# Kernel optimization log

Hardware: AMD Instinct MI355X
Metric: run time of the kernel (lower is better)

## Reference

```python
import math
import jax, jax.numpy as jnp
import numpy as np

N_MARKS = 64
D_TYPE = 256      # d_type_emb (= d_k since each head module has n_head=1)
D_TIME = 256      # must be even
N_HEAD = 4
N_LAYERS = 3
D_IN = D_TYPE + D_TIME  # input dim to per-layer QKV projections
NEG = -1000000000.0
LN_EPS = 1e-5


def temporal_embedding(time):
    # time: [B,T] -> [B,T,D_TIME]; pe[...,0::2]=sin(t*div), pe[...,1::2]=cos(t*div)
    div_term = jnp.exp(jnp.arange(0, D_TIME, 2, dtype=time.dtype) * (-(math.log(10000.0) / D_TIME)))
    ang = time[..., None] * div_term  # [B,T,D_TIME//2]
    pe = jnp.stack([jnp.sin(ang), jnp.cos(ang)], axis=-1)  # interleave sin/cos
    return pe.reshape(time.shape[0], time.shape[1], D_TIME)


def layer_norm(x, w, b):
    mu = jnp.mean(x, axis=-1, keepdims=True)
    var = jnp.mean(jnp.square(x - mu), axis=-1, keepdims=True)
    return (x - mu) * jax.lax.rsqrt(var + LN_EPS) * w + b


def setup_inputs() -> dict:
    key = jax.random.key(0)
    ks = jax.random.split(key, 12)
    B, T = 4, 1024
    event_seqs = jax.random.uniform(ks[0], (B, T, N_MARKS), dtype=jnp.float32)
    time_seqs = jax.random.uniform(ks[1], (B, T), dtype=jnp.float32)
    non_pad_mask = jnp.ones((B, T, T), dtype=bool)
    s_in = 1.0 / math.sqrt(D_IN)
    s_mk = 1.0 / math.sqrt(N_MARKS)
    Wtype = jax.random.uniform(ks[2], (N_MARKS, D_TYPE), minval=-s_mk, maxval=s_mk)
    btype = jax.random.uniform(ks[3], (D_TYPE,), minval=-s_mk, maxval=s_mk)
    Wq = jax.random.uniform(ks[4], (N_HEAD, N_LAYERS, D_IN, D_TYPE), minval=-s_in, maxval=s_in)
    bq = jax.random.uniform(ks[5], (N_HEAD, N_LAYERS, D_TYPE), minval=-s_in, maxval=s_in)
    Wk = jax.random.uniform(ks[6], (N_HEAD, N_LAYERS, D_IN, D_TYPE), minval=-s_in, maxval=s_in)
    bk = jax.random.uniform(ks[7], (N_HEAD, N_LAYERS, D_TYPE), minval=-s_in, maxval=s_in)
    Wv = jax.random.uniform(ks[8], (N_HEAD, N_LAYERS, D_IN, D_TYPE), minval=-s_in, maxval=s_in)
    bv = jax.random.uniform(ks[9], (N_HEAD, N_LAYERS, D_TYPE), minval=-s_in, maxval=s_in)
    norm_w = jnp.ones((D_TYPE,), dtype=jnp.float32)
    norm_b = jnp.zeros((D_TYPE,), dtype=jnp.float32)
    return {"event_seqs": event_seqs, "time_seqs": time_seqs, "non_pad_mask": non_pad_mask,
            "Wtype": Wtype, "btype": btype, "Wq": Wq, "bq": bq, "Wk": Wk, "bk": bk,
            "Wv": Wv, "bv": bv, "norm_w": norm_w, "norm_b": norm_b}


def reference(event_seqs, time_seqs, non_pad_mask, Wtype, btype, Wq, bq, Wk, bk, Wv, bv, norm_w, norm_b):
    B, T, _ = event_seqs.shape
    # attention mask: True => masked (torch masked_fill(mask > 0, -1e9)); strict+diag upper tri
    tri = jnp.triu(jnp.ones((T, T), dtype=bool))[None]           # [1,T,T]
    attention_mask = tri & non_pad_mask                          # [B,T,T]
    layer_mask = jnp.broadcast_to(~jnp.eye(T, dtype=bool)[None], (B, T, T))
    top = jnp.concatenate([attention_mask, jnp.ones((B, T, T), dtype=bool)], axis=-1)
    bot = jnp.concatenate([attention_mask, layer_mask], axis=-1)
    combined_mask = jnp.concatenate([top, bot], axis=1)          # [B,2T,2T]

    time_emb = temporal_embedding(time_seqs)                     # [B,T,D_TIME]
    type_emb = jnp.tanh(event_seqs @ Wtype + btype)              # [B,T,D_TYPE]
    event_emb = jnp.concatenate([type_emb, time_emb], axis=-1)   # [B,T,D_IN]
    sample_time_emb = time_emb                                   # sample_times=None path
    init_cur = jnp.zeros_like(type_emb)

    scale = 1.0 / math.sqrt(D_TYPE)
    cur_layers = []
    # NOTE: event_emb is sequentially updated across layers AND heads, matching the source.
    for h in range(N_HEAD):
        cur = init_cur
        for l in range(N_LAYERS):
            x = jnp.concatenate([event_emb,
                                 jnp.concatenate([cur, sample_time_emb], axis=-1)], axis=1)  # [B,2T,D_IN]
            q = x @ Wq[h, l] + bq[h, l]
            k = x @ Wk[h, l] + bk[h, l]
            v = x @ Wv[h, l] + bv[h, l]
            scores = jnp.einsum('bqd,bkd->bqk', q, k) * scale    # [B,2T,2T]
            scores = jnp.where(combined_mask, NEG, scores)
            p = jax.nn.softmax(scores, axis=-1)
            out = jnp.einsum('bqk,bkd->bqd', p, v)               # [B,2T,D_TYPE]
            cur = jnp.tanh(out[:, T:, :]) + cur
            event_emb = jnp.concatenate([out[:, :T, :], time_emb], axis=-1)
            cur = layer_norm(cur, norm_w, norm_b)                # use_norm=True
        cur_layers.append(cur)
    return jnp.concatenate(cur_layers, axis=-1)                  # [B,T,D_TYPE*N_HEAD]
```

## Files before the change

### kernel.cpp

```cpp
#include <hip/hip_runtime.h>

typedef __attribute__((ext_vector_type(8))) short short8;
typedef __attribute__((ext_vector_type(4))) float f32x4;
typedef __attribute__((ext_vector_type(4))) unsigned short us4v;
typedef unsigned short ushort_t;
typedef unsigned int uint_t;

#define BB 4
#define T_ 1024
#define T2 2048
#define DD 256
#define DIN 512
#define NMARK 64
#define LNEPS 1e-5f
#define KDIV (-0.035977892078032f)
#define SEGL 8

__device__ __forceinline__ ushort_t f2bf(float f) {
  unsigned int u = __float_as_uint(f);
  unsigned int r = (u + 0x7fffu + ((u >> 16) & 1u)) >> 16;
  return (ushort_t)r;
}
__device__ __forceinline__ uint_t pack2(float a, float b) {
  return (uint_t)f2bf(a) | ((uint_t)f2bf(b) << 16);
}
__device__ __forceinline__ uint_t cvtpk(float lo, float hi) {
  uint_t r;
  asm("v_cvt_pk_bf16_f32 %0, %1, %2" : "=v"(r) : "v"(lo), "v"(hi));
  return r;
}

typedef const __attribute__((address_space(1))) unsigned int* as1cu32;
typedef __attribute__((address_space(3))) unsigned int* as3u32;
__device__ __forceinline__ void async_copy16(const void* g, void* l) {
  __builtin_amdgcn_global_load_lds((as1cu32)g, (as3u32)l, 16, 0, 0);
}

__global__ __launch_bounds__(256) void k_init(const float* __restrict__ ev,
                                              const float* __restrict__ tm,
                                              const float* __restrict__ Wt,
                                              const float* __restrict__ bt,
                                              ushort_t* __restrict__ Xh,
                                              float* __restrict__ Cur) {
  const int btq = blockIdx.x;
  const int b = btq >> 10;
  const int t = btq & 1023;
  const int d = threadIdx.x;
  __shared__ float evs[NMARK];
  if (d < NMARK) evs[d] = ev[(size_t)btq * NMARK + d];
  __syncthreads();
  float s = bt[d];
#pragma unroll
  for (int m = 0; m < NMARK; ++m) s += evs[m] * Wt[m * DD + d];
  const float te_type = tanhf(s);
  const float tv = tm[btq];
  const int i = d >> 1;
  const float dv = expf((float)(2 * i) * KDIV);
  const float ang = tv * dv;
  const float te_time = (d & 1) ? cosf(ang) : sinf(ang);
  ushort_t* Xb = Xh + (size_t)b * T2 * DIN;
  const ushort_t tt = f2bf(te_time);
  Xb[(size_t)t * DIN + d] = f2bf(te_type);
  Xb[(size_t)t * DIN + DD + d] = tt;
  Xb[(size_t)(T_ + t) * DIN + d] = 0;
  Xb[(size_t)(T_ + t) * DIN + DD + d] = tt;
  Cur[((size_t)b * T_ + t) * DD + d] = 0.0f;
}

__global__ __launch_bounds__(256) void k_transW(const float* __restrict__ Wq,
                                                const float* __restrict__ Wk,
                                                const float* __restrict__ Wv,
                                                ushort_t* __restrict__ WT) {
  const int mi = blockIdx.x;
  const int wsel = mi / 12, hl = mi % 12;
  const float* W = ((wsel == 0) ? Wq : (wsel == 1) ? Wk : Wv) + (size_t)hl * DIN * DD;
  const int t = blockIdx.y;
  const int k0 = (t >> 2) * 64, n0 = (t & 3) * 64;
  __shared__ float Ts[64][65];
  const int tid = threadIdx.x;
#pragma unroll
  for (int i = 0; i < 16; ++i) {
    const int idx = tid + i * 256;
    const int r = idx >> 6, c = idx & 63;
    Ts[r][c] = W[(size_t)(k0 + r) * DD + n0 + c];
  }
  __syncthreads();
  ushort_t* D = WT + (size_t)mi * DD * DIN;
#pragma unroll
  for (int i = 0; i < 16; ++i) {
    const int idx = tid + i * 256;
    const int rn = idx >> 6, ck = idx & 63;
    D[(size_t)(n0 + rn) * DIN + k0 + ck] = f2bf(Ts[ck][rn]);
  }
}

__global__ __launch_bounds__(256) void k_qkv(const ushort_t* __restrict__ Xh,
                                             const ushort_t* __restrict__ WT,
                                             const float* __restrict__ bq,
                                             const float* __restrict__ bk,
                                             const float* __restrict__ bv,
                                             ushort_t* __restrict__ Qh,
                                             ushort_t* __restrict__ Kh,
                                             ushort_t* __restrict__ VTt,
                                             int hl) {
  const int m0 = blockIdx.x * 128;
  const int n0 = blockIdx.y * 128;
  const int wsel = blockIdx.z;
  const ushort_t* Bt = WT + ((size_t)(wsel * 12 + hl)) * DD * DIN + (size_t)n0 * DIN;
  const float* bias = (wsel == 0) ? bq : (wsel == 1) ? bk : bv;

  __shared__ ushort_t As[128 * 64];
  __shared__ ushort_t Bs[128 * 64];
  const int tid = threadIdx.x;
  const int w = tid >> 6, lane = tid & 63;
  const int wr = w >> 1, wc = w & 1;
  const int lr = lane & 15, kg = lane >> 4;

  f32x4 acc[4][4];
  const f32x4 z4 = {0.f, 0.f, 0.f, 0.f};
#pragma unroll
  for (int a = 0; a < 4; ++a)
#pragma unroll
    for (int c = 0; c < 4; ++c) acc[a][c] = z4;

  for (int k0 = 0; k0 < DIN; k0 += 64) {
#pragma unroll
    for (int i = 0; i < 4; ++i) {
      const int idx = tid + i * 256;
      const int row = idx >> 3, ch = idx & 7;
      const int db = row * 128 + ((ch * 16) ^ ((row & 7) << 4));
      uint4 va = *(const uint4*)&Xh[(size_t)(m0 + row) * DIN + k0 + ch * 8];
      *(uint4*)((char*)As + db) = va;
      uint4 vb = *(const uint4*)&Bt[(size_t)row * DIN + k0 + ch * 8];
      *(uint4*)((char*)Bs + db) = vb;
    }
    __syncthreads();
#pragma unroll
    for (int kk = 0; kk < 2; ++kk) {
      short8 af[4], bfr[4];
      const int cb = kk * 64 + kg * 16;
#pragma unroll
      for (int mi = 0; mi < 4; ++mi) {
        const int row = wr * 64 + mi * 16 + lr;
        af[mi] = *(const short8*)((const char*)As + row * 128 + (cb ^ ((row & 7) << 4)));
      }
#pragma unroll
      for (int ni = 0; ni < 4; ++ni) {
        const int row = wc * 64 + ni * 16 + lr;
        bfr[ni] = *(const short8*)((const char*)Bs + row * 128 + (cb ^ ((row & 7) << 4)));
      }
#pragma unroll
      for (int mi = 0; mi < 4; ++mi)
#pragma unroll
        for (int ni = 0; ni < 4; ++ni)
          acc[mi][ni] = __builtin_amdgcn_mfma_f32_16x16x32_bf16(af[mi], bfr[ni], acc[mi][ni], 0, 0, 0);
    }
    __syncthreads();
  }

  if (wsel < 2) {
    ushort_t* C = (wsel == 0) ? Qh : Kh;
#pragma unroll
    for (int mi = 0; mi < 4; ++mi)
#pragma unroll
      for (int ni = 0; ni < 4; ++ni) {
        const int col = n0 + wc * 64 + ni * 16 + lr;
        const float bcol = bias[col];
        const int rbase = m0 + wr * 64 + mi * 16 + kg * 4;
#pragma unroll
        for (int r = 0; r < 4; ++r)
          C[(size_t)(rbase + r) * DD + col] = f2bf(acc[mi][ni][r] + bcol);
      }
  } else {
    const int b2 = m0 >> 11;
    const int t0q = m0 & 2047;
#pragma unroll
    for (int mi = 0; mi < 4; ++mi)
#pragma unroll
      for (int ni = 0; ni < 4; ++ni) {
        const int col = n0 + wc * 64 + ni * 16 + lr;
        const float bcol = bias[col];
        const int t32 = (t0q >> 5) + wr * 2 + (mi >> 1);
        const int jloc = kg * 8 + (mi & 1) * 4;
        uint2 pk;
        pk.x = pack2(acc[mi][ni][0] + bcol, acc[mi][ni][1] + bcol);
        pk.y = pack2(acc[mi][ni][2] + bcol, acc[mi][ni][3] + bcol);
        *(uint2*)(VTt + ((size_t)(b2 * 64 + t32)) * (DD * 32) + col * 32 + jloc) = pk;
      }
  }
}

__global__ __launch_bounds__(128, 1) void k_fpart(const ushort_t* __restrict__ Qh,
                                                  const ushort_t* __restrict__ Kh,
                                                  const ushort_t* __restrict__ VTt,
                                                  float* __restrict__ PartO,
                                                  float* __restrict__ PartML) {
  __shared__ char lds[65536];
  const int tid = threadIdx.x;
  const int bx = blockIdx.x;
  const int r = bx & 255;
  const int seg = bx >> 8;
  const int hb = r & 1;
  const int b = (r >> 1) & 3;
  const int tc = 31 - (r >> 3);
  const int nt = tc + 1 + hb;
  const int nseg = (nt + SEGL - 1) / SEGL;
  if (seg >= nseg) return;
  const int kt0 = seg * SEGL;
  const int klen = (nt - kt0 < SEGL) ? (nt - kt0) : SEGL;
  const int t0 = tc * 32;
  const int nc = tc + 1;
  const int dt = 32 + tc;

  const int w = tid >> 6, lane = tid & 63;
  const int kg = lane >> 4, lr = lane & 15;
  const int tloc = w * 16 + lr;
  const int t = t0 + tloc;
  const int r0 = (hb ? T_ : 0) + t;
  const size_t bT2 = (size_t)b * T2;

  short8 qf[8];
  {
    const ushort_t* qb = Qh + (bT2 + r0) * DD + kg * 8;
#pragma unroll
    for (int kk = 0; kk < 8; ++kk) qf[kk] = *(const short8*)(qb + kk * 32);
  }

  const f32x4 z4 = {0.f, 0.f, 0.f, 0.f};
  f32x4 acc_o[16];
#pragma unroll
  for (int db = 0; db < 16; ++db) acc_o[db] = z4;
  float m_run = -1e30f, l_run = 0.f;

#define STAGE(BUF, TILE)                                                                  \
  {                                                                                       \
    const int _t = (TILE);                                                                \
    const char* Vt = (const char*)VTt + ((size_t)(b * 64 + _t)) * 16384;                  \
    _Pragma("unroll") for (int s = 0; s < 8; ++s) {                                       \
      const int row2 = (w * 8 + s) * 2 + (lane >> 5);                                     \
      const int cc2 = lane & 31;                                                          \
      async_copy16((const char*)Kh + ((bT2 + _t * 32 + row2) * DD) * 2 +                  \
                       ((cc2 * 16) ^ ((row2 & 7) << 4)),                                  \
                   lds + (BUF) * 16384 + (w * 8 + s) * 1024);                             \
      async_copy16(Vt + (w * 8 + s) * 1024 + (lane << 4),                                 \
                   lds + 32768 + (BUF) * 16384 + (w * 8 + s) * 1024);                     \
    }                                                                                     \
  }
#define TILEOF(KT) (((KT) < nc) ? (KT) : dt)

  STAGE(0, TILEOF(kt0));

  union U8 { uint4 u; short8 s; };

  for (int ktl = 0; ktl < klen; ++ktl) {
    const int kt = kt0 + ktl;
    const int tile = TILEOF(kt);
    const bool isDiag = (kt >= nc);

    if (ktl + 1 < klen) {
      STAGE((ktl + 1) & 1, TILEOF(kt + 1));
      asm volatile("s_waitcnt vmcnt(16)" ::: "memory");
    } else {
      asm volatile("s_waitcnt vmcnt(0)" ::: "memory");
    }
    __builtin_amdgcn_s_barrier();
    asm volatile("" ::: "memory");

    const char* KsC = lds + (ktl & 1) * 16384;
    const char* VsC = lds + 32768 + (ktl & 1) * 16384;

    f32x4 sa[2];
#pragma unroll
    for (int jb = 0; jb < 2; ++jb) {
      sa[jb] = z4;
      const int rowj = jb * 16 + lr;
      const int base = rowj * 512;
      const int swj = (rowj & 7) << 4;
#pragma unroll
      for (int kk = 0; kk < 8; ++kk) {
        short8 kf = *(const short8*)(KsC + base + ((kk * 64 + kg * 16) ^ swj));
        sa[jb] = __builtin_amdgcn_mfma_f32_16x16x32_bf16(kf, qf[kk], sa[jb], 0, 0, 0);
      }
    }

    float sv[8];
    float tmax = -1e30f;
#pragma unroll
    for (int jb = 0; jb < 2; ++jb)
#pragma unroll
      for (int rr = 0; rr < 4; ++rr) {
        const int jl = jb * 16 + kg * 4 + rr;
        const bool valid = isDiag ? (jl == tloc) : ((tile * 32 + jl) < t);
        const float x = valid ? sa[jb][rr] * 0.0625f : -1e30f;
        sv[jb * 4 + rr] = x;
        tmax = fmaxf(tmax, x);
      }
    tmax = fmaxf(tmax, __shfl_xor(tmax, 16, 64));
    tmax = fmaxf(tmax, __shfl_xor(tmax, 32, 64));
    if (tmax > m_run + 8.0f) {
      const float fac = __expf(m_run - tmax);
      m_run = tmax;
      l_run *= fac;
#pragma unroll
      for (int db = 0; db < 16; ++db) acc_o[db] *= fac;
    }
    float p[8];
    float psum = 0.f;
#pragma unroll
    for (int e = 0; e < 8; ++e) {
      const float pe = (sv[e] > -1e29f) ? __expf(sv[e] - m_run) : 0.0f;
      p[e] = pe;
      psum += pe;
    }
    psum += __shfl_xor(psum, 16, 64);
    psum += __shfl_xor(psum, 32, 64);
    l_run += psum;

    U8 pf;
    pf.u.x = cvtpk(p[0], p[1]);
    pf.u.y = cvtpk(p[2], p[3]);
    pf.u.z = cvtpk(p[4], p[5]);
    pf.u.w = cvtpk(p[6], p[7]);

#pragma unroll
    for (int db = 0; db < 16; ++db) {
      U8 vf;
      vf.u = *(const uint4*)(VsC + (db * 16 + lr) * 64 + kg * 16);
      acc_o[db] = __builtin_amdgcn_mfma_f32_16x16x32_bf16(vf.s, pf.s, acc_o[db], 0, 0, 0);
    }

    __builtin_amdgcn_s_barrier();
    asm volatile("" ::: "memory");
  }
#undef STAGE
#undef TILEOF

  float* pml = PartML + (r * 5 + seg) * 64;
  if (kg == 0) { pml[tloc] = m_run; pml[32 + tloc] = l_run; }
  float* po = PartO + ((size_t)(r * 5 + seg)) * (32 * 256) + tloc * 256 + kg * 4;
#pragma unroll
  for (int db = 0; db < 16; ++db) *(f32x4*)(po + db * 16) = acc_o[db];
}

__global__ __launch_bounds__(128) void k_merge(const ushort_t* __restrict__ VTt,
                                               float* __restrict__ Cur,
                                               ushort_t* __restrict__ Xh,
                                               float* __restrict__ out,
                                               const float* __restrict__ nw,
                                               const float* __restrict__ nb,
                                               const float* __restrict__ PartO,
                                               const float* __restrict__ PartML,
                                               int lastLayer, int h) {
  __shared__ float red[128];
  const int tid = threadIdx.x;
  const int r = blockIdx.x;
  const int hb = r & 1;
  const int b = (r >> 1) & 3;
  const int tc = 31 - (r >> 3);
  const int nt = tc + 1 + hb;
  const int nseg = (nt + SEGL - 1) / SEGL;
  const int t0 = tc * 32;

  const int w = tid >> 6, lane = tid & 63;
  const int kg = lane >> 4, lr = lane & 15;
  const int tloc = w * 16 + lr;
  const int t = t0 + tloc;
  const size_t bT2 = (size_t)b * T2;
  const f32x4 z4 = {0.f, 0.f, 0.f, 0.f};

  float mstar = -1e30f;
  for (int s = 0; s < nseg; ++s)
    mstar = fmaxf(mstar, PartML[(r * 5 + s) * 64 + tloc]);
  float l_run = 0.f;
  f32x4 acc_o[16];
#pragma unroll
  for (int db = 0; db < 16; ++db) acc_o[db] = z4;
  for (int s = 0; s < nseg; ++s) {
    const float* pml = PartML + (r * 5 + s) * 64;
    const float f = __expf(pml[tloc] - mstar);
    l_run += f * pml[32 + tloc];
    const float* po = PartO + ((size_t)(r * 5 + s)) * (32 * 256) + tloc * 256 + kg * 4;
#pragma unroll
    for (int db = 0; db < 16; ++db) {
      f32x4 v = *(const f32x4*)(po + db * 16);
#pragma unroll
      for (int q = 0; q < 4; ++q) acc_o[db][q] += f * v[q];
    }
  }

  const float oinv = 1.0f / l_run;

  if (!hb) {
    if (t != 0) {
      ushort_t* xp = Xh + (bT2 + t) * DIN + kg * 4;
#pragma unroll
      for (int db = 0; db < 16; ++db) {
        us4v o;
#pragma unroll
        for (int rr = 0; rr < 4; ++rr) o[rr] = f2bf(acc_o[db][rr] * oinv);
        *(us4v*)(xp + db * 16) = o;
      }
    }
  } else {
    float* cp = Cur + ((size_t)b * T_ + t) * DD + kg * 4;
    float s1 = 0.f, s2 = 0.f;
#pragma unroll
    for (int db = 0; db < 16; ++db) {
      f32x4 c4 = *(const f32x4*)(cp + db * 16);
#pragma unroll
      for (int rr = 0; rr < 4; ++rr) {
        const float x = tanhf(acc_o[db][rr] * oinv) + c4[rr];
        acc_o[db][rr] = x;
        s1 += x;
        s2 += x * x;
      }
    }
    s1 += __shfl_xor(s1, 16, 64); s1 += __shfl_xor(s1, 32, 64);
    s2 += __shfl_xor(s2, 16, 64); s2 += __shfl_xor(s2, 32, 64);
    const float mean = s1 * (1.0f / 256.0f);
    const float var = s2 * (1.0f / 256.0f) - mean * mean;
    const float rinv = rsqrtf(var + LNEPS);
    ushort_t* xp = Xh + (bT2 + T_ + t) * DIN + kg * 4;
    if (lastLayer) {
      float* op = out + ((size_t)b * T_ + t) * (DD * 4) + h * DD + kg * 4;
      const us4v zz = {0, 0, 0, 0};
      const f32x4 zf = {0.f, 0.f, 0.f, 0.f};
#pragma unroll
      for (int db = 0; db < 16; ++db) {
        f32x4 w4 = *(const f32x4*)&nw[db * 16 + kg * 4];
        f32x4 b4 = *(const f32x4*)&nb[db * 16 + kg * 4];
        f32x4 y;
#pragma unroll
        for (int rr = 0; rr < 4; ++rr) y[rr] = (acc_o[db][rr] - mean) * rinv * w4[rr] + b4[rr];
        *(f32x4*)(op + db * 16) = y;
        *(f32x4*)(cp + db * 16) = zf;
        *(us4v*)(xp + db * 16) = zz;
      }
    } else {
#pragma unroll
      for (int db = 0; db < 16; ++db) {
        f32x4 w4 = *(const f32x4*)&nw[db * 16 + kg * 4];
        f32x4 b4 = *(const f32x4*)&nb[db * 16 + kg * 4];
        f32x4 y;
        us4v yh;
#pragma unroll
        for (int rr = 0; rr < 4; ++rr) {
          y[rr] = (acc_o[db][rr] - mean) * rinv * w4[rr] + b4[rr];
          yh[rr] = f2bf(y[rr]);
        }
        *(f32x4*)(cp + db * 16) = y;
        *(us4v*)(xp + db * 16) = yh;
      }
    }
  }

  if (!hb && tc < 4) {
    const int col = tc * 64 + (tid & 63);
    const int half = tid >> 6;
    float s = 0.f;
    for (int tl = half * 32; tl < half * 32 + 32; ++tl) {
      const ushort_t* vp = VTt + ((size_t)(b * 64 + tl)) * 8192 + col * 32;
#pragma unroll
      for (int j = 0; j < 32; j += 8) {
        uint4 v = *(const uint4*)(vp + j);
        const uint_t vs[4] = {v.x, v.y, v.z, v.w};
#pragma unroll
        for (int q = 0; q < 4; ++q) {
          s += __uint_as_float(vs[q] << 16);
          s += __uint_as_float(vs[q] & 0xffff0000u);
        }
      }
    }
    red[half * 64 + (tid & 63)] = s;
    __syncthreads();
    if (tid < 64)
      Xh[bT2 * DIN + tc * 64 + tid] =
          f2bf((red[tid] + red[64 + tid]) * (1.0f / 2048.0f));
  }
}

extern "C" void kernel_launch(void* const* d_in, const int* in_sizes, int n_in,
                              void* d_out, int out_size, void* d_ws, size_t ws_size,
                              hipStream_t stream) {
  const float* ev = (const float*)d_in[0];
  const float* tm = (const float*)d_in[1];
  const float* Wt = (const float*)d_in[3];
  const float* bt = (const float*)d_in[4];
  const float* Wq = (const float*)d_in[5];
  const float* bq = (const float*)d_in[6];
  const float* Wk = (const float*)d_in[7];
  const float* bk = (const float*)d_in[8];
  const float* Wv = (const float*)d_in[9];
  const float* bv = (const float*)d_in[10];
  const float* nw = (const float*)d_in[11];
  const float* nb = (const float*)d_in[12];
  float* out = (float*)d_out;

  char* p = (char*)d_ws;
  ushort_t* Xh  = (ushort_t*)p; p += (size_t)BB * T2 * DIN * 2;
  ushort_t* Qh  = (ushort_t*)p; p += (size_t)BB * T2 * DD * 2;
  ushort_t* Kh  = (ushort_t*)p; p += (size_t)BB * T2 * DD * 2;
  ushort_t* VTt = (ushort_t*)p; p += (size_t)BB * T2 * DD * 2;
  float* Cur    = (float*)p;    p += (size_t)BB * T_ * DD * 4;
  ushort_t* WT  = (ushort_t*)p; p += (size_t)36 * DD * DIN * 2;
  float* PartO  = (float*)p;    p += (size_t)256 * 5 * 32 * 256 * 4;
  float* PartML = (float*)p;

  k_init<<<BB * T_, 256, 0, stream>>>(ev, tm, Wt, bt, Xh, Cur);
  k_transW<<<dim3(36, 32), 256, 0, stream>>>(Wq, Wk, Wv, WT);

  for (int h = 0; h < 4; ++h) {
    for (int l = 0; l < 3; ++l) {
      const int hl = h * 3 + l;
      const size_t boff = (size_t)hl * DD;
      k_qkv<<<dim3(64, 2, 3), 256, 0, stream>>>(Xh, WT, bq + boff, bk + boff, bv + boff,
                                                Qh, Kh, VTt, hl);
      k_fpart<<<1280, 128, 0, stream>>>(Qh, Kh, VTt, PartO, PartML);
      k_merge<<<256, 128, 0, stream>>>(VTt, Cur, Xh, out, nw, nb,
                                       PartO, PartML, (l == 2) ? 1 : 0, h);
    }
  }
}
```

Before: 783.8 us.

## Share K/V tiles across both query halves and fuse single-segment epilogue into attention

Each attention block now covers the event half and the sample half of the same 32-row query chunk with 4 waves, so each staged K/V tile in LDS is loaded once and used by both halves. The event-half waves skip the diagonal tile. Blocks that need only one key segment finish the tanh/layernorm epilogue inline, which removes the partial-result writes and the merge work for short rows. The merge kernel now runs only on chunks with several segments. The larger blocks and the epilogue code inside the attention kernel may raise register pressure and reduce occupancy.

```diff
diff --git a/kernel.cpp b/kernel.cpp
--- a/kernel.cpp
+++ b/kernel.cpp
@@ -190,33 +190,37 @@
   }
 }
 
-__global__ __launch_bounds__(128, 1) void k_fpart(const ushort_t* __restrict__ Qh,
+__global__ __launch_bounds__(256, 2) void k_fpart(const ushort_t* __restrict__ Qh,
                                                   const ushort_t* __restrict__ Kh,
                                                   const ushort_t* __restrict__ VTt,
+                                                  float* __restrict__ Cur,
+                                                  ushort_t* __restrict__ Xh,
+                                                  float* __restrict__ out,
+                                                  const float* __restrict__ nw,
+                                                  const float* __restrict__ nb,
                                                   float* __restrict__ PartO,
-                                                  float* __restrict__ PartML) {
-  __shared__ char lds[65536];
+                                                  float* __restrict__ PartML,
+                                                  int lastLayer, int h) {
+  __shared__ char lds[66560];
   const int tid = threadIdx.x;
   const int bx = blockIdx.x;
-  const int r = bx & 255;
-  const int seg = bx >> 8;
-  const int hb = r & 1;
-  const int b = (r >> 1) & 3;
-  const int tc = 31 - (r >> 3);
-  const int nt = tc + 1 + hb;
+  const int seg = bx >> 7;
+  const int rem = bx & 127;
+  const int b = rem & 3;
+  const int tc = 31 - (rem >> 2);
+  const int nt = tc + 2;
   const int nseg = (nt + SEGL - 1) / SEGL;
   if (seg >= nseg) return;
   const int kt0 = seg * SEGL;
   const int klen = (nt - kt0 < SEGL) ? (nt - kt0) : SEGL;
-  const int t0 = tc * 32;
-  const int nc = tc + 1;
   const int dt = 32 + tc;
 
   const int w = tid >> 6, lane = tid & 63;
   const int kg = lane >> 4, lr = lane & 15;
-  const int tloc = w * 16 + lr;
-  const int t = t0 + tloc;
-  const int r0 = (hb ? T_ : 0) + t;
+  const int half = w >> 1;
+  const int tq = (w & 1) * 16 + lr;
+  const int t = tc * 32 + tq;
+  const int r0 = (half ? T_ : 0) + t;
   const size_t bT2 = (size_t)b * T2;
 
   short8 qf[8];
@@ -236,17 +240,18 @@
   {                                                                                       \
     const int _t = (TILE);                                                                \
     const char* Vt = (const char*)VTt + ((size_t)(b * 64 + _t)) * 16384;                  \
-    _Pragma("unroll") for (int s = 0; s < 8; ++s) {                                       \
-      const int row2 = (w * 8 + s) * 2 + (lane >> 5);                                     \
+    _Pragma("unroll") for (int s = 0; s < 4; ++s) {                                       \
+      const int c = w * 4 + s;                                                            \
+      const int row2 = (c << 1) | (lane >> 5);                                            \
       const int cc2 = lane & 31;                                                          \
       async_copy16((const char*)Kh + ((bT2 + _t * 32 + row2) * DD) * 2 +                  \
                        ((cc2 * 16) ^ ((row2 & 7) << 4)),                                  \
-                   lds + (BUF) * 16384 + (w * 8 + s) * 1024);                             \
-      async_copy16(Vt + (w * 8 + s) * 1024 + (lane << 4),                                 \
-                   lds + 32768 + (BUF) * 16384 + (w * 8 + s) * 1024);                     \
+                   lds + (BUF) * 16384 + c * 1024);                                       \
+      async_copy16(Vt + c * 1024 + lane * 16,                                             \
+                   lds + 32768 + (BUF) * 16384 + c * 1024);                               \
     }                                                                                     \
   }
-#define TILEOF(KT) (((KT) < nc) ? (KT) : dt)
+#define TILEOF(KT) (((KT) <= tc) ? (KT) : dt)
 
   STAGE(0, TILEOF(kt0));
 
@@ -255,78 +260,80 @@
   for (int ktl = 0; ktl < klen; ++ktl) {
     const int kt = kt0 + ktl;
     const int tile = TILEOF(kt);
-    const bool isDiag = (kt >= nc);
+    const bool isDiag = (kt > tc);
 
     if (ktl + 1 < klen) {
       STAGE((ktl + 1) & 1, TILEOF(kt + 1));
-      asm volatile("s_waitcnt vmcnt(16)" ::: "memory");
+      asm volatile("s_waitcnt vmcnt(8)" ::: "memory");
     } else {
       asm volatile("s_waitcnt vmcnt(0)" ::: "memory");
     }
     __builtin_amdgcn_s_barrier();
     asm volatile("" ::: "memory");
 
-    const char* KsC = lds + (ktl & 1) * 16384;
-    const char* VsC = lds + 32768 + (ktl & 1) * 16384;
-
-    f32x4 sa[2];
-#pragma unroll
-    for (int jb = 0; jb < 2; ++jb) {
-      sa[jb] = z4;
-      const int rowj = jb * 16 + lr;
-      const int base = rowj * 512;
-      const int swj = (rowj & 7) << 4;
-#pragma unroll
-      for (int kk = 0; kk < 8; ++kk) {
-        short8 kf = *(const short8*)(KsC + base + ((kk * 64 + kg * 16) ^ swj));
-        sa[jb] = __builtin_amdgcn_mfma_f32_16x16x32_bf16(kf, qf[kk], sa[jb], 0, 0, 0);
-      }
-    }
-
-    float sv[8];
-    float tmax = -1e30f;
-#pragma unroll
-    for (int jb = 0; jb < 2; ++jb)
-#pragma unroll
-      for (int rr = 0; rr < 4; ++rr) {
-        const int jl = jb * 16 + kg * 4 + rr;
-        const bool valid = isDiag ? (jl == tloc) : ((tile * 32 + jl) < t);
-        const float x = valid ? sa[jb][rr] * 0.0625f : -1e30f;
-        sv[jb * 4 + rr] = x;
-        tmax = fmaxf(tmax, x);
-      }
-    tmax = fmaxf(tmax, __shfl_xor(tmax, 16, 64));
-    tmax = fmaxf(tmax, __shfl_xor(tmax, 32, 64));
-    if (tmax > m_run + 8.0f) {
-      const float fac = __expf(m_run - tmax);
-      m_run = tmax;
-      l_run *= fac;
-#pragma unroll
-      for (int db = 0; db < 16; ++db) acc_o[db] *= fac;
-    }
-    float p[8];
-    float psum = 0.f;
-#pragma unroll
-    for (int e = 0; e < 8; ++e) {
-      const float pe = (sv[e] > -1e29f) ? __expf(sv[e] - m_run) : 0.0f;
-      p[e] = pe;
-      psum += pe;
-    }
-    psum += __shfl_xor(psum, 16, 64);
-    psum += __shfl_xor(psum, 32, 64);
-    l_run += psum;
-
-    U8 pf;
-    pf.u.x = cvtpk(p[0], p[1]);
-    pf.u.y = cvtpk(p[2], p[3]);
-    pf.u.z = cvtpk(p[4], p[5]);
-    pf.u.w = cvtpk(p[6], p[7]);
-
-#pragma unroll
-    for (int db = 0; db < 16; ++db) {
-      U8 vf;
-      vf.u = *(const uint4*)(VsC + (db * 16 + lr) * 64 + kg * 16);
-      acc_o[db] = __builtin_amdgcn_mfma_f32_16x16x32_bf16(vf.s, pf.s, acc_o[db], 0, 0, 0);
+    if (!(isDiag && half == 0)) {
+      const char* KsC = lds + (ktl & 1) * 16384;
+      const char* VsC = lds + 32768 + (ktl & 1) * 16384;
+
+      f32x4 sa[2];
+#pragma unroll
+      for (int jb = 0; jb < 2; ++jb) {
+        sa[jb] = z4;
+        const int rowj = jb * 16 + lr;
+        const int base = rowj * 512;
+        const int swj = (rowj & 7) << 4;
+#pragma unroll
+        for (int kk = 0; kk < 8; ++kk) {
+          short8 kf = *(const short8*)(KsC + base + ((kk * 64 + kg * 16) ^ swj));
+          sa[jb] = __builtin_amdgcn_mfma_f32_16x16x32_bf16(kf, qf[kk], sa[jb], 0, 0, 0);
+        }
+      }
+
+      float sv[8];
+      float tmax = -1e30f;
+#pragma unroll
+      for (int jb = 0; jb < 2; ++jb)
+#pragma unroll
+        for (int rr = 0; rr < 4; ++rr) {
+          const int jl = jb * 16 + kg * 4 + rr;
+          const bool valid = isDiag ? (jl == tq) : ((tile * 32 + jl) < t);
+          const float x = valid ? sa[jb][rr] * 0.0625f : -1e30f;
+          sv[jb * 4 + rr] = x;
+          tmax = fmaxf(tmax, x);
+        }
+      tmax = fmaxf(tmax, __shfl_xor(tmax, 16, 64));
+      tmax = fmaxf(tmax, __shfl_xor(tmax, 32, 64));
+      if (tmax > m_run + 8.0f) {
+        const float fac = __expf(m_run - tmax);
+        m_run = tmax;
+        l_run *= fac;
+#pragma unroll
+        for (int db = 0; db < 16; ++db) acc_o[db] *= fac;
+      }
+      float p[8];
+      float psum = 0.f;
+#pragma unroll
+      for (int e = 0; e < 8; ++e) {
+        const float pe = (sv[e] > -1e29f) ? __expf(sv[e] - m_run) : 0.0f;
+        p[e] = pe;
+        psum += pe;
+      }
+      psum += __shfl_xor(psum, 16, 64);
+      psum += __shfl_xor(psum, 32, 64);
+      l_run += psum;
+
+      U8 pf;
+      pf.u.x = cvtpk(p[0], p[1]);
+      pf.u.y = cvtpk(p[2], p[3]);
+      pf.u.z = cvtpk(p[4], p[5]);
+      pf.u.w = cvtpk(p[6], p[7]);
+
+#pragma unroll
+      for (int db = 0; db < 16; ++db) {
+        U8 vf;
+        vf.u = *(const uint4*)(VsC + (db * 16 + lr) * 64 + kg * 16);
+        acc_o[db] = __builtin_amdgcn_mfma_f32_16x16x32_bf16(vf.s, pf.s, acc_o[db], 0, 0, 0);
+      }
     }
 
     __builtin_amdgcn_s_barrier();
@@ -335,62 +342,20 @@
 #undef STAGE
 #undef TILEOF
 
-  float* pml = PartML + (r * 5 + seg) * 64;
-  if (kg == 0) { pml[tloc] = m_run; pml[32 + tloc] = l_run; }
-  float* po = PartO + ((size_t)(r * 5 + seg)) * (32 * 256) + tloc * 256 + kg * 4;
-#pragma unroll
-  for (int db = 0; db < 16; ++db) *(f32x4*)(po + db * 16) = acc_o[db];
-}
-
-__global__ __launch_bounds__(128) void k_merge(const ushort_t* __restrict__ VTt,
-                                               float* __restrict__ Cur,
-                                               ushort_t* __restrict__ Xh,
-                                               float* __restrict__ out,
-                                               const float* __restrict__ nw,
-                                               const float* __restrict__ nb,
-                                               const float* __restrict__ PartO,
-                                               const float* __restrict__ PartML,
-                                               int lastLayer, int h) {
-  __shared__ float red[128];
-  const int tid = threadIdx.x;
-  const int r = blockIdx.x;
-  const int hb = r & 1;
-  const int b = (r >> 1) & 3;
-  const int tc = 31 - (r >> 3);
-  const int nt = tc + 1 + hb;
-  const int nseg = (nt + SEGL - 1) / SEGL;
-  const int t0 = tc * 32;
-
-  const int w = tid >> 6, lane = tid & 63;
-  const int kg = lane >> 4, lr = lane & 15;
-  const int tloc = w * 16 + lr;
-  const int t = t0 + tloc;
-  const size_t bT2 = (size_t)b * T2;
-  const f32x4 z4 = {0.f, 0.f, 0.f, 0.f};
-
-  float mstar = -1e30f;
-  for (int s = 0; s < nseg; ++s)
-    mstar = fmaxf(mstar, PartML[(r * 5 + s) * 64 + tloc]);
-  float l_run = 0.f;
-  f32x4 acc_o[16];
-#pragma unroll
-  for (int db = 0; db < 16; ++db) acc_o[db] = z4;
-  for (int s = 0; s < nseg; ++s) {
-    const float* pml = PartML + (r * 5 + s) * 64;
-    const float f = __expf(pml[tloc] - mstar);
-    l_run += f * pml[32 + tloc];
-    const float* po = PartO + ((size_t)(r * 5 + s)) * (32 * 256) + tloc * 256 + kg * 4;
-#pragma unroll
-    for (int db = 0; db < 16; ++db) {
-      f32x4 v = *(const f32x4*)(po + db * 16);
-#pragma unroll
-      for (int q = 0; q < 4; ++q) acc_o[db][q] += f * v[q];
-    }
+  if (nseg > 1) {
+    const int slot = (b * 32 + tc) * 5 + seg;
+    const int row = half * 32 + tq;
+    float* pml = PartML + slot * 128;
+    if (kg == 0) { pml[row] = m_run; pml[64 + row] = l_run; }
+    float* po = PartO + ((size_t)slot) * (64 * 256) + row * 256 + kg * 4;
+#pragma unroll
+    for (int db = 0; db < 16; ++db) *(f32x4*)(po + db * 16) = acc_o[db];
+    return;
   }
 
   const float oinv = 1.0f / l_run;
 
-  if (!hb) {
+  if (!half) {
     if (t != 0) {
       ushort_t* xp = Xh + (bT2 + t) * DIN + kg * 4;
 #pragma unroll
@@ -454,11 +419,13 @@
     }
   }
 
-  if (!hb && tc < 4) {
+  if (tc < 4) {
+    __syncthreads();
+    float* red = (float*)(lds + 65536);
     const int col = tc * 64 + (tid & 63);
-    const int half = tid >> 6;
+    const int q4 = tid >> 6;
     float s = 0.f;
-    for (int tl = half * 32; tl < half * 32 + 32; ++tl) {
+    for (int tl = q4 * 16; tl < q4 * 16 + 16; ++tl) {
       const ushort_t* vp = VTt + ((size_t)(b * 64 + tl)) * 8192 + col * 32;
 #pragma unroll
       for (int j = 0; j < 32; j += 8) {
@@ -471,11 +438,121 @@
         }
       }
     }
-    red[half * 64 + (tid & 63)] = s;
+    red[q4 * 64 + (tid & 63)] = s;
     __syncthreads();
     if (tid < 64)
       Xh[bT2 * DIN + tc * 64 + tid] =
-          f2bf((red[tid] + red[64 + tid]) * (1.0f / 2048.0f));
+          f2bf((red[tid] + red[64 + tid] + red[128 + tid] + red[192 + tid]) * (1.0f / 2048.0f));
+  }
+}
+
+__global__ __launch_bounds__(256) void k_merge(float* __restrict__ Cur,
+                                               ushort_t* __restrict__ Xh,
+                                               float* __restrict__ out,
+                                               const float* __restrict__ nw,
+                                               const float* __restrict__ nb,
+                                               const float* __restrict__ PartO,
+                                               const float* __restrict__ PartML,
+                                               int lastLayer, int h) {
+  const int tid = threadIdx.x;
+  const int bx = blockIdx.x;
+  const int b = bx & 3;
+  const int tc = 7 + (bx >> 2);
+  const int nt = tc + 2;
+  const int nseg = (nt + SEGL - 1) / SEGL;
+  const int slot0 = (b * 32 + tc) * 5;
+
+  const int w = tid >> 6, lane = tid & 63;
+  const int kg = lane >> 4, lr = lane & 15;
+  const int half = w >> 1;
+  const int tq = (w & 1) * 16 + lr;
+  const int t = tc * 32 + tq;
+  const int row = half * 32 + tq;
+  const size_t bT2 = (size_t)b * T2;
+  const f32x4 z4 = {0.f, 0.f, 0.f, 0.f};
+
+  float mstar = -1e30f;
+  for (int s = 0; s < nseg; ++s)
+    mstar = fmaxf(mstar, PartML[(slot0 + s) * 128 + row]);
+  float l_run = 0.f;
+  f32x4 acc_o[16];
+#pragma unroll
+  for (int db = 0; db < 16; ++db) acc_o[db] = z4;
+  for (int s = 0; s < nseg; ++s) {
+    const float* pml = PartML + (slot0 + s) * 128;
+    const float f = __expf(pml[row] - mstar);
+    l_run += f * pml[64 + row];
+    const float* po = PartO + ((size_t)(slot0 + s)) * (64 * 256) + row * 256 + kg * 4;
+#pragma unroll
+    for (int db = 0; db < 16; ++db) {
+      f32x4 v = *(const f32x4*)(po + db * 16);
+#pragma unroll
+      for (int q = 0; q < 4; ++q) acc_o[db][q] += f * v[q];
+    }
+  }
+
+  const float oinv = 1.0f / l_run;
+
+  if (!half) {
+    ushort_t* xp = Xh + (bT2 + t) * DIN + kg * 4;
+#pragma unroll
+    for (int db = 0; db < 16; ++db) {
+      us4v o;
+#pragma unroll
+      for (int rr = 0; rr < 4; ++rr) o[rr] = f2bf(acc_o[db][rr] * oinv);
+      *(us4v*)(xp + db * 16) = o;
+    }
+  } else {
+    float* cp = Cur + ((size_t)b * T_ + t) * DD + kg * 4;
+    float s1 = 0.f, s2 = 0.f;
+#pragma unroll
+    for (int db = 0; db < 16; ++db) {
+      f32x4 c4 = *(const f32x4*)(cp + db * 16);
+#pragma unroll
+      for (int rr = 0; rr < 4; ++rr) {
+        const float x = tanhf(acc_o[db][rr] * oinv) + c4[rr];
+        acc_o[db][rr] = x;
+        s1 += x;
+        s2 += x * x;
+      }
+    }
+    s1 += __shfl_xor(s1, 16, 64); s1 += __shfl_xor(s1, 32, 64);
+    s2 += __shfl_xor(s2, 16, 64); s2 += __shfl_xor(s2, 32, 64);
+    const float mean = s1 * (1.0f / 256.0f);
+    const float var = s2 * (1.0f / 256.0f) - mean * mean;
+    const float rinv = rsqrtf(var + LNEPS);
+    ushort_t* xp = Xh + (bT2 + T_ + t) * DIN + kg * 4;
+    if (lastLayer) {
+      float* op = out + ((size_t)b * T_ + t) * (DD * 4) + h * DD + kg * 4;
+      const us4v zz = {0, 0, 0, 0};
+      const f32x4 zf = {0.f, 0.f, 0.f, 0.f};
+#pragma unroll
+      for (int db = 0; db < 16; ++db) {
+        f32x4 w4 = *(const f32x4*)&nw[db * 16 + kg * 4];
+        f32x4 b4 = *(const f32x4*)&nb[db * 16 + kg * 4];
+        f32x4 y;
+#pragma unroll
+        for (int rr = 0; rr < 4; ++rr) y[rr] = (acc_o[db][rr] - mean) * rinv * w4[rr] + b4[rr];
+        *(f32x4*)(op + db * 16) = y;
+        *(f32x4*)(cp + db * 16) = zf;
+        *(us4v*)(xp + db * 16) = zz;
+      }
+    } else {
+#pragma unroll
+      for (int db = 0; db < 16; ++db) {
+        f32x4 w4 = *(const f32x4*)&nw[db * 16 + kg * 4];
+        f32x4 b4 = *(const f32x4*)&nb[db * 16 + kg * 4];
+        f32x4 y;
+        us4v yh;
+#pragma unroll
+        for (int rr = 0; rr < 4; ++rr) {
+          y[rr] = (acc_o[db][rr] - mean) * rinv * w4[rr] + b4[rr];
+          yh[rr] = f2bf(y[rr]);
+        }
+        *(f32x4*)(cp + db * 16) = y;
+        *(us4v*)(xp + db * 16) = yh;
+      }
+    }
   }
 }
 
@@ -503,7 +580,7 @@
   ushort_t* VTt = (ushort_t*)p; p += (size_t)BB * T2 * DD * 2;
   float* Cur    = (float*)p;    p += (size_t)BB * T_ * DD * 4;
   ushort_t* WT  = (ushort_t*)p; p += (size_t)36 * DD * DIN * 2;
-  float* PartO  = (float*)p;    p += (size_t)256 * 5 * 32 * 256 * 4;
+  float* PartO  = (float*)p;    p += (size_t)640 * 64 * 256 * 4;
   float* PartML = (float*)p;
 
   k_init<<<BB * T_, 256, 0, stream>>>(ev, tm, Wt, bt, Xh, Cur);
@@ -515,9 +592,10 @@
       const size_t boff = (size_t)hl * DD;
       k_qkv<<<dim3(64, 2, 3), 256, 0, stream>>>(Xh, WT, bq + boff, bk + boff, bv + boff,
                                                 Qh, Kh, VTt, hl);
-      k_fpart<<<1280, 128, 0, stream>>>(Qh, Kh, VTt, PartO, PartML);
-      k_merge<<<256, 128, 0, stream>>>(VTt, Cur, Xh, out, nw, nb,
+      k_fpart<<<640, 256, 0, stream>>>(Qh, Kh, VTt, Cur, Xh, out, nw, nb,
                                        PartO, PartML, (l == 2) ? 1 : 0, h);
-    }
-  }
-}
+      k_merge<<<100, 256, 0, stream>>>(Cur, Xh, out, nw, nb,
+                                       PartO, PartML, (l == 2) ? 1 : 0, h);
+    }
+  }
+}
```

New measurement: 755.7 us. -3.6%, faster.
